# Kernel tuning notes

Hardware: AMD Instinct MI355X
Metric: run time of the kernel (lower is better)

Reference implementation:

```python
import jax, jax.numpy as jnp
import numpy as np

REDUCTION_SIZE = 2


def setup_inputs() -> dict:
    key = jax.random.key(0)
    k1, k2 = jax.random.split(key)
    T, E, K, D = 32768, 256, 8, 8  # tokens, experts, top-k, devices
    topk_tensor = jax.random.normal(k1, (1, 1, T, E), dtype=jnp.float32)
    # one-hot expert -> device mapping (contiguous blocks of E//D experts per device)
    dev_of_expert = jnp.arange(E, dtype=jnp.int32) // (E // D)
    expert_mapping = jax.nn.one_hot(dev_of_expert, D, dtype=jnp.int32)[None, None]  # [1,1,E,D]
    expert_metadata = jax.random.randint(k2, (1, 1, T, K), 0, E, dtype=jnp.int32)[None][0]
    return {
        "topk_tensor": topk_tensor,
        "expert_mapping": expert_mapping,
        "expert_metadata": expert_metadata,
    }


def reference(topk_tensor, expert_mapping, expert_metadata):
    r = REDUCTION_SIZE
    topk = topk_tensor[0, 0]          # [T, E] scores over all experts
    mapping = expert_mapping[0, 0]    # [E, D] one-hot expert->device
    meta = expert_metadata[0, 0]      # [T, K] selected expert indices
    T, E = topk.shape
    D = mapping.shape[-1]

    dev_of_expert = jnp.argmax(mapping, axis=-1)            # [E]
    tok_dev = dev_of_expert[meta]                           # [T, K] device of each selected expert

    # token -> device dispatch mask, reduced over groups of `r` tokens
    rows = jnp.arange(T, dtype=jnp.int32)[:, None]
    mask = jnp.zeros((T, D), dtype=jnp.int32).at[rows, tok_dev].set(1)  # [T, D]
    reduced_mask = mask.reshape(T // r, r, D).max(axis=1)               # [T//r, D]

    # selection mask over experts (scatter, avoids [T,K,E] one-hot blowup)
    sel = jnp.zeros((T, E), dtype=topk.dtype).at[rows, meta].set(1.0)   # [T, E]
    gated = topk * sel                                                  # zero non-selected scores

    # remap expert columns into device-local slots
    perm = jnp.argsort(dev_of_expert, stable=True)                      # experts grouped by device
    remapped = gated[:, perm].reshape(T, D, E // D).transpose(1, 0, 2)  # [D, T, E//D]
    return remapped, reduced_mask
```

## Files before the change

### kernel.cpp

```cpp
#include <hip/hip_runtime.h>

#define T_TOK 32768
#define E_EXP 256
#define K_SEL 8
#define D_DEV 8
#define SLOTS (E_EXP / D_DEV)
#define NBLK  2048
#define TOK_PER_BLK 16
#define ROWP 264

typedef float floatx4 __attribute__((ext_vector_type(4)));

__global__ __launch_bounds__(256, 8) void moe_fused_kernel(
    const float* __restrict__ topk, const int* __restrict__ mapping,
    const int* __restrict__ meta, float* __restrict__ out_remap,
    float* __restrict__ out_mask) {
  __shared__ float tile[TOK_PER_BLK * ROWP];
  __shared__ int sdev[E_EXP];
  __shared__ int spos[E_EXP];
  __shared__ int scnt[4 * D_DEV];

  const int tid  = threadIdx.x;
  const int w    = tid >> 6;
  const int lane = tid & 63;
  const int tbase = blockIdx.x * TOK_PER_BLK;

  int e = 0;
  if (tid < 128) e = meta[(size_t)tbase * K_SEL + tid];

  const int4 m0 = ((const int4*)mapping)[tid * 2];
  const int4 m1 = ((const int4*)mapping)[tid * 2 + 1];

  const floatx4 z4 = {0.f, 0.f, 0.f, 0.f};
#pragma unroll
  for (int i = 0; i < 4; ++i) {
    const int fid = i * 256 + tid;
    const int a = ((fid >> 3) & 15) * ROWP + (fid >> 7) * SLOTS + (fid & 7) * 4;
    *(floatx4*)&tile[a] = z4;
  }

  {
    int vals[8] = {m0.x, m0.y, m0.z, m0.w, m1.x, m1.y, m1.z, m1.w};
    int best = vals[0], dev = 0;
#pragma unroll
    for (int d = 1; d < 8; ++d)
      if (vals[d] > best) { best = vals[d]; dev = d; }
    sdev[tid] = dev;

    unsigned long long myball = 0ull;
#pragma unroll
    for (int d = 0; d < 8; ++d) {
      unsigned long long b = __ballot(dev == d);
      if (d == dev) myball = b;
      if (lane == d) scnt[w * 8 + d] = __popcll(b);
    }
    const unsigned long long lt = (lane == 0) ? 0ull : (~0ull >> (64 - lane));
    const int lower = __popcll(myball & lt);
    __syncthreads();
    int base = 0;
    for (int d = 0; d < dev; ++d)
      base += scnt[0 * 8 + d] + scnt[1 * 8 + d] + scnt[2 * 8 + d] +
              scnt[3 * 8 + d];
    for (int w2 = 0; w2 < w; ++w2) base += scnt[w2 * 8 + dev];
    spos[tid] = base + lower;
    __syncthreads();
  }

  if (tid < 128) {
    const int tl  = (w << 3) + (lane >> 3);
    const float sc = topk[(size_t)(tbase + tl) * E_EXP + e];
    const int pos = spos[e];
    const int dv  = sdev[e];

    unsigned long long bsel = 0ull;
#pragma unroll
    for (int d = 0; d < D_DEV; ++d) {
      unsigned long long b = __ballot(dv == d);
      if ((lane & 7) == d) bsel = b;
    }
    if (lane < 32) {
      const float fm =
          ((bsel >> (16 * (lane >> 3))) & 0xFFFFull) ? 1.0f : 0.0f;
      const int rowi = (tbase >> 1) + (w << 2) + (lane >> 3);
      out_mask[(size_t)rowi * D_DEV + (lane & 7)] = fm;
    }

    tile[tl * ROWP + pos] = sc;
  }
  __syncthreads();

#pragma unroll
  for (int i = 0; i < 4; ++i) {
    const int fid = i * 256 + tid;
    const int t      = (fid >> 3) & 15;
    const int dchunk = fid >> 7;
    const int j      = (fid & 7) * 4;
    const floatx4 v = *(const floatx4*)&tile[t * ROWP + dchunk * SLOTS + j];
    float* dst = out_remap + (size_t)dchunk * T_TOK * SLOTS +
                 (size_t)(tbase + t) * SLOTS + j;
    __builtin_nontemporal_store(v, (floatx4*)dst);
  }
}

extern "C" void kernel_launch(void* const* d_in, const int* in_sizes, int n_in,
                              void* d_out, int out_size, void* d_ws, size_t ws_size,
                              hipStream_t stream) {
  const float* topk    = (const float*)d_in[0];
  const int*   mapping = (const int*)d_in[1];
  const int*   meta    = (const int*)d_in[2];

  float* out_remap = (float*)d_out;
  float* out_mask  = out_remap + (size_t)D_DEV * T_TOK * SLOTS;

  moe_fused_kernel<<<NBLK, 256, 0, stream>>>(topk, mapping, meta, out_remap,
                                             out_mask);
}
```

Baseline: 87.40 us.

## Split into zero-fill kernel plus direct scatter of selected scores

Replaces the fused kernel, which staged a zeroed LDS tile and wrote dense vec4 rows, with two kernels. The first bulk-zeroes the remapped output. The second, now handling 32 tokens per block with all 256 threads active, scatters each selected score directly to global memory and writes the dispatch mask. This drops the LDS tile and one block barrier, but adds a second launch, a separate full-output write pass, and scattered 4-byte stores into lines the zero pass already wrote.

```diff
diff --git a/kernel.cpp b/kernel.cpp
--- a/kernel.cpp
+++ b/kernel.cpp
@@ -5,17 +5,24 @@
 #define K_SEL 8
 #define D_DEV 8
 #define SLOTS (E_EXP / D_DEV)
-#define NBLK  2048
-#define TOK_PER_BLK 16
-#define ROWP 264
+#define TOK_PER_BLK 32
 
 typedef float floatx4 __attribute__((ext_vector_type(4)));
 
-__global__ __launch_bounds__(256, 8) void moe_fused_kernel(
+__global__ __launch_bounds__(256) void zero_remap_kernel(
+    float* __restrict__ out_remap) {
+  const size_t i = (size_t)blockIdx.x * 256 + threadIdx.x;
+  const floatx4 z4 = {0.f, 0.f, 0.f, 0.f};
+  floatx4* o = (floatx4*)out_remap;
+#pragma unroll
+  for (int r = 0; r < 4; ++r)
+    o[i + (size_t)r * (2048u * 256u)] = z4;
+}
+
+__global__ __launch_bounds__(256) void scatter_kernel(
     const float* __restrict__ topk, const int* __restrict__ mapping,
     const int* __restrict__ meta, float* __restrict__ out_remap,
     float* __restrict__ out_mask) {
-  __shared__ float tile[TOK_PER_BLK * ROWP];
   __shared__ int sdev[E_EXP];
   __shared__ int spos[E_EXP];
   __shared__ int scnt[4 * D_DEV];
@@ -24,20 +31,13 @@
   const int w    = tid >> 6;
   const int lane = tid & 63;
   const int tbase = blockIdx.x * TOK_PER_BLK;
+  const int tl = tid >> 3;
 
-  int e = 0;
-  if (tid < 128) e = meta[(size_t)tbase * K_SEL + tid];
+  const int e = meta[(size_t)tbase * K_SEL + tid];
+  const float sc = topk[(size_t)(tbase + tl) * E_EXP + e];
 
   const int4 m0 = ((const int4*)mapping)[tid * 2];
   const int4 m1 = ((const int4*)mapping)[tid * 2 + 1];
-
-  const floatx4 z4 = {0.f, 0.f, 0.f, 0.f};
-#pragma unroll
-  for (int i = 0; i < 4; ++i) {
-    const int fid = i * 256 + tid;
-    const int a = ((fid >> 3) & 15) * ROWP + (fid >> 7) * SLOTS + (fid & 7) * 4;
-    *(floatx4*)&tile[a] = z4;
-  }
 
   {
     int vals[8] = {m0.x, m0.y, m0.z, m0.w, m1.x, m1.y, m1.z, m1.w};
@@ -63,15 +63,13 @@
               scnt[3 * 8 + d];
     for (int w2 = 0; w2 < w; ++w2) base += scnt[w2 * 8 + dev];
     spos[tid] = base + lower;
-    __syncthreads();
   }
+  __syncthreads();
 
-  if (tid < 128) {
-    const int tl  = (w << 3) + (lane >> 3);
-    const float sc = topk[(size_t)(tbase + tl) * E_EXP + e];
-    const int pos = spos[e];
-    const int dv  = sdev[e];
+  const int pos = spos[e];
+  const int dv  = sdev[e];
 
+  {
     unsigned long long bsel = 0ull;
 #pragma unroll
     for (int d = 0; d < D_DEV; ++d) {
@@ -84,22 +82,11 @@
       const int rowi = (tbase >> 1) + (w << 2) + (lane >> 3);
       out_mask[(size_t)rowi * D_DEV + (lane & 7)] = fm;
     }
+  }
 
-    tile[tl * ROWP + pos] = sc;
-  }
-  __syncthreads();
-
-#pragma unroll
-  for (int i = 0; i < 4; ++i) {
-    const int fid = i * 256 + tid;
-    const int t      = (fid >> 3) & 15;
-    const int dchunk = fid >> 7;
-    const int j      = (fid & 7) * 4;
-    const floatx4 v = *(const floatx4*)&tile[t * ROWP + dchunk * SLOTS + j];
-    float* dst = out_remap + (size_t)dchunk * T_TOK * SLOTS +
-                 (size_t)(tbase + t) * SLOTS + j;
-    __builtin_nontemporal_store(v, (floatx4*)dst);
-  }
+  float* dst = out_remap + (size_t)(pos >> 5) * T_TOK * SLOTS +
+               (size_t)(tbase + tl) * SLOTS + (pos & 31);
+  __builtin_nontemporal_store(sc, dst);
 }
 
 extern "C" void kernel_launch(void* const* d_in, const int* in_sizes, int n_in,
@@ -112,6 +99,7 @@
   float* out_remap = (float*)d_out;
   float* out_mask  = out_remap + (size_t)D_DEV * T_TOK * SLOTS;
 
-  moe_fused_kernel<<<NBLK, 256, 0, stream>>>(topk, mapping, meta, out_remap,
-                                             out_mask);
+  zero_remap_kernel<<<2048, 256, 0, stream>>>(out_remap);
+  scatter_kernel<<<T_TOK / TOK_PER_BLK, 256, 0, stream>>>(
+      topk, mapping, meta, out_remap, out_mask);
 }
```

Result: slower. 90.55 us (+3.6%).

## Assign one wavefront per token and build output rows via shuffles

Applied to the files above, without the earlier changes.

Blocks now cover 4 tokens instead of 16, with one wavefront per token. The shared-memory tile, its zeroing and one barrier are removed. Each lane assembles its 16-byte output chunk in registers by shuffling the 8 selected (position, score) pairs across the wave. The reduced mask is built from per-wave ballots combined through a small shared array. The trade-off is that the expert-to-device permutation setup, including the mapping load, ballots and a barrier, is now repeated in four times as many blocks.

```diff
diff --git a/kernel.cpp b/kernel.cpp
--- a/kernel.cpp
+++ b/kernel.cpp
@@ -5,9 +5,8 @@
 #define K_SEL 8
 #define D_DEV 8
 #define SLOTS (E_EXP / D_DEV)
-#define NBLK  2048
-#define TOK_PER_BLK 16
-#define ROWP 264
+#define NBLK  8192
+#define TOK_PER_BLK 4
 
 typedef float floatx4 __attribute__((ext_vector_type(4)));
 
@@ -15,31 +14,26 @@
     const float* __restrict__ topk, const int* __restrict__ mapping,
     const int* __restrict__ meta, float* __restrict__ out_remap,
     float* __restrict__ out_mask) {
-  __shared__ float tile[TOK_PER_BLK * ROWP];
   __shared__ int sdev[E_EXP];
   __shared__ int spos[E_EXP];
   __shared__ int scnt[4 * D_DEV];
+  __shared__ int smask[4];
 
   const int tid  = threadIdx.x;
   const int w    = tid >> 6;
   const int lane = tid & 63;
-  const int tbase = blockIdx.x * TOK_PER_BLK;
+  const int t    = blockIdx.x * TOK_PER_BLK + w;
 
   int e = 0;
-  if (tid < 128) e = meta[(size_t)tbase * K_SEL + tid];
-
-  const int4 m0 = ((const int4*)mapping)[tid * 2];
-  const int4 m1 = ((const int4*)mapping)[tid * 2 + 1];
-
-  const floatx4 z4 = {0.f, 0.f, 0.f, 0.f};
-#pragma unroll
-  for (int i = 0; i < 4; ++i) {
-    const int fid = i * 256 + tid;
-    const int a = ((fid >> 3) & 15) * ROWP + (fid >> 7) * SLOTS + (fid & 7) * 4;
-    *(floatx4*)&tile[a] = z4;
+  float sc = 0.0f;
+  if (lane < 8) {
+    e  = meta[(size_t)t * K_SEL + lane];
+    sc = topk[(size_t)t * E_EXP + e];
   }
 
   {
+    const int4 m0 = ((const int4*)mapping)[tid * 2];
+    const int4 m1 = ((const int4*)mapping)[tid * 2 + 1];
     int vals[8] = {m0.x, m0.y, m0.z, m0.w, m1.x, m1.y, m1.z, m1.w};
     int best = vals[0], dev = 0;
 #pragma unroll
@@ -63,42 +57,44 @@
               scnt[3 * 8 + d];
     for (int w2 = 0; w2 < w; ++w2) base += scnt[w2 * 8 + dev];
     spos[tid] = base + lower;
-    __syncthreads();
-  }
-
-  if (tid < 128) {
-    const int tl  = (w << 3) + (lane >> 3);
-    const float sc = topk[(size_t)(tbase + tl) * E_EXP + e];
-    const int pos = spos[e];
-    const int dv  = sdev[e];
-
-    unsigned long long bsel = 0ull;
-#pragma unroll
-    for (int d = 0; d < D_DEV; ++d) {
-      unsigned long long b = __ballot(dv == d);
-      if ((lane & 7) == d) bsel = b;
-    }
-    if (lane < 32) {
-      const float fm =
-          ((bsel >> (16 * (lane >> 3))) & 0xFFFFull) ? 1.0f : 0.0f;
-      const int rowi = (tbase >> 1) + (w << 2) + (lane >> 3);
-      out_mask[(size_t)rowi * D_DEV + (lane & 7)] = fm;
-    }
-
-    tile[tl * ROWP + pos] = sc;
   }
   __syncthreads();
 
+  int pos = 0, dv = 8;
+  if (lane < 8) {
+    pos = spos[e];
+    dv  = sdev[e];
+  }
+
+  float4 row = {0.f, 0.f, 0.f, 0.f};
 #pragma unroll
-  for (int i = 0; i < 4; ++i) {
-    const int fid = i * 256 + tid;
-    const int t      = (fid >> 3) & 15;
-    const int dchunk = fid >> 7;
-    const int j      = (fid & 7) * 4;
-    const floatx4 v = *(const floatx4*)&tile[t * ROWP + dchunk * SLOTS + j];
-    float* dst = out_remap + (size_t)dchunk * T_TOK * SLOTS +
-                 (size_t)(tbase + t) * SLOTS + j;
-    __builtin_nontemporal_store(v, (floatx4*)dst);
+  for (int g = 0; g < 8; ++g) {
+    const int   pg = __shfl(pos, g, 64);
+    const float sg = __shfl(sc, g, 64);
+    const bool mine = (pg >> 2) == lane;
+    const int c = pg & 3;
+    row.x = (mine && c == 0) ? sg : row.x;
+    row.y = (mine && c == 1) ? sg : row.y;
+    row.z = (mine && c == 2) ? sg : row.z;
+    row.w = (mine && c == 3) ? sg : row.w;
+  }
+
+  float* dst = out_remap + (size_t)(lane >> 3) * T_TOK * SLOTS +
+               (size_t)t * SLOTS + (lane & 7) * 4;
+  __builtin_nontemporal_store(*(floatx4*)&row, (floatx4*)dst);
+
+  unsigned dmask = 0;
+#pragma unroll
+  for (int d = 0; d < D_DEV; ++d) {
+    const unsigned long long b = __ballot(dv == d);
+    dmask |= (b ? 1u : 0u) << d;
+  }
+  if (lane == 0) smask[w] = (int)dmask;
+  __syncthreads();
+  if ((w & 1) == 0 && lane < 8) {
+    const unsigned comb = (unsigned)smask[w] | (unsigned)smask[w + 1];
+    out_mask[(size_t)(t >> 1) * D_DEV + lane] =
+        ((comb >> lane) & 1u) ? 1.0f : 0.0f;
   }
 }
 
```

Measured after the change: 94.32 us. 7.9% more time.
